# Optimization experiments

Measured on AMD Instinct MI355X. Metric: run time of the kernel, lower is better.

The kernel has to match this reference:

```python
import jax, jax.numpy as jnp
import numpy as np

DIM = 1024
N_EXPERTS = 8
TOP_K = 2
EXPERT_HIDDEN = DIM * 2
B, T = 4, 4096


def setup_inputs() -> dict:
    key = jax.random.key(0)
    ks = jax.random.split(key, 5)
    # xavier_uniform with gain=0.02 for w1/w2 (fan_in=DIM, fan_out=EXPERT_HIDDEN)
    lim12 = 0.02 * np.sqrt(6.0 / (DIM + EXPERT_HIDDEN))
    lim3 = 0.02 * np.sqrt(6.0 / (EXPERT_HIDDEN + DIM))
    x = jax.random.normal(ks[0], (B, T, DIM), dtype=jnp.float32)
    router_w = 0.02 * jax.random.normal(ks[1], (N_EXPERTS, DIM), dtype=jnp.float32)
    w1 = jax.random.uniform(ks[2], (N_EXPERTS, DIM, EXPERT_HIDDEN), minval=-lim12, maxval=lim12, dtype=jnp.float32)
    w2 = jax.random.uniform(ks[3], (N_EXPERTS, DIM, EXPERT_HIDDEN), minval=-lim12, maxval=lim12, dtype=jnp.float32)
    w3 = jax.random.uniform(ks[4], (N_EXPERTS, EXPERT_HIDDEN, DIM), minval=-lim3, maxval=lim3, dtype=jnp.float32)
    return {"x": x, "router_w": router_w, "w1": w1, "w2": w2, "w3": w3}


def reference(x, router_w, w1, w2, w3):
    # Router: top-k softmax gating, renormalized over the selected k.
    logits = jnp.einsum('btd,ed->bte', x, router_w)          # [B,T,E]
    probs = jax.nn.softmax(logits, axis=-1)
    topk_vals, topk_idx = jax.lax.top_k(probs, TOP_K)        # [B,T,K]
    topk_weights = topk_vals / topk_vals.sum(axis=-1, keepdims=True)

    out = jnp.zeros_like(x)
    for e in range(N_EXPERTS):
        # gate weight for expert e per token (0 if e not in token's top-k)
        w_e = jnp.where(topk_idx == e, topk_weights, 0.0).sum(axis=-1)  # [B,T]
        h = jax.nn.silu(jnp.einsum('btd,dh->bth', x, w1[e])) * jnp.einsum('btd,dh->bth', x, w2[e])
        out = out + jnp.einsum('bth,hd->btd', h, w3[e]) * w_e[..., None]
    aux_loss = jnp.float32(0.0)  # eval mode
    return (out, aux_loss)
```

## Files before the change

kernel.cpp:

```cpp
#include <hip/hip_runtime.h>
#include <stdint.h>

#define TTOK 16384
#define NDIM 1024
#define NHID 2048
#define NEXP 8
#define TM 256
#define MAXT 136
#define SLOTCAP (2 * TTOK + NEXP * TM)

typedef __attribute__((ext_vector_type(8))) short short8;
typedef __attribute__((ext_vector_type(4))) float f32x4;

__device__ __forceinline__ unsigned short f2bf(float f) {
  unsigned int u = __float_as_uint(f);
  u += 0x7FFFu + ((u >> 16) & 1u);
  return (unsigned short)(u >> 16);
}

__device__ __forceinline__ void gload16(const void* g, void* l) {
  __builtin_amdgcn_global_load_lds(
      (const __attribute__((address_space(1))) unsigned int*)g,
      (__attribute__((address_space(3))) unsigned int*)l, 16, 0, 0);
}

__device__ __forceinline__ float silu(float z) {
  return z / (1.0f + __expf(-z));
}

__device__ __forceinline__ void router_block(int b, const float* __restrict__ x,
                                             const float* __restrict__ rw,
                                             unsigned short* __restrict__ xbf,
                                             int* __restrict__ tok_e,
                                             float* __restrict__ tok_gw) {
  int t = (b << 2) + (threadIdx.x >> 6);
  int lane = threadIdx.x & 63;
  const float4* xr = (const float4*)(x + (size_t)t * NDIM);

  float4 v[4];
  float d[NEXP];
#pragma unroll
  for (int e = 0; e < NEXP; ++e) d[e] = 0.f;

#pragma unroll
  for (int i = 0; i < 4; ++i) {
    int c = i * 64 + lane;
    v[i] = xr[c];
#pragma unroll
    for (int e = 0; e < NEXP; ++e) {
      float4 w = ((const float4*)(rw + e * NDIM))[c];
      d[e] += v[i].x * w.x + v[i].y * w.y + v[i].z * w.z + v[i].w * w.w;
    }
  }
#pragma unroll
  for (int e = 0; e < NEXP; ++e)
    for (int s = 32; s; s >>= 1) d[e] += __shfl_xor(d[e], s, 64);

  unsigned short* xo = xbf + (size_t)t * NDIM;
#pragma unroll
  for (int i = 0; i < 4; ++i) {
    int c = i * 64 + lane;
    ushort4 u;
    u.x = f2bf(v[i].x); u.y = f2bf(v[i].y); u.z = f2bf(v[i].z); u.w = f2bf(v[i].w);
    ((ushort4*)xo)[c] = u;
  }

  if (lane == 0) {
    float m = d[0];
#pragma unroll
    for (int e = 1; e < NEXP; ++e) m = fmaxf(m, d[e]);
    float ex[NEXP];
#pragma unroll
    for (int e = 0; e < NEXP; ++e) ex[e] = __expf(d[e] - m);
    int e0 = 0;
#pragma unroll
    for (int e = 1; e < NEXP; ++e) if (ex[e] > ex[e0]) e0 = e;
    int e1 = (e0 == 0) ? 1 : 0;
#pragma unroll
    for (int e = 0; e < NEXP; ++e) if (e != e0 && ex[e] > ex[e1]) e1 = e;
    float p0 = ex[e0], p1 = ex[e1];
    float inv = 1.f / (p0 + p1);
    tok_e[2 * t] = e0; tok_e[2 * t + 1] = e1;
    tok_gw[2 * t] = p0 * inv; tok_gw[2 * t + 1] = p1 * inv;
  }
}

__device__ __forceinline__ void tconv_tile(const float* __restrict__ src,
                                           unsigned short* __restrict__ dst,
                                           int R, int C, int bx, int by) {
  __shared__ unsigned short tile[64][65];
  int tx = threadIdx.x & 15, ty = threadIdx.x >> 4;
#pragma unroll
  for (int rr = 0; rr < 4; ++rr) {
    int rl = rr * 16 + ty;
    float4 v = *(const float4*)(src + (size_t)(by + rl) * C + bx + tx * 4);
    tile[rl][tx * 4 + 0] = f2bf(v.x);
    tile[rl][tx * 4 + 1] = f2bf(v.y);
    tile[rl][tx * 4 + 2] = f2bf(v.z);
    tile[rl][tx * 4 + 3] = f2bf(v.w);
  }
  __syncthreads();
#pragma unroll
  for (int rr = 0; rr < 4; ++rr) {
    int cl = rr * 16 + ty;
    ushort4 u;
    u.x = tile[tx * 4 + 0][cl];
    u.y = tile[tx * 4 + 1][cl];
    u.z = tile[tx * 4 + 2][cl];
    u.w = tile[tx * 4 + 3][cl];
    *(ushort4*)(dst + (size_t)(bx + cl) * R + by + tx * 4) = u;
  }
}

__global__ void k_prep(const float* __restrict__ x, const float* __restrict__ rw,
                       unsigned short* __restrict__ xbf, int* __restrict__ tok_e,
                       float* __restrict__ tok_gw, const float* __restrict__ w1,
                       const float* __restrict__ w2, const float* __restrict__ w3,
                       unsigned short* __restrict__ w1t, unsigned short* __restrict__ w2t,
                       unsigned short* __restrict__ w3t) {
  int b = blockIdx.x;
  if (b < 4096) {
    router_block(b, x, rw, xbf, tok_e, tok_gw);
    return;
  }
  int tcb = b - 4096;
  int bx = tcb & 31;
  int by = (tcb >> 5) & 15;
  int z = tcb >> 9;
  if (z < 16) {
    int e = z & 7;
    const float* src = (z < 8 ? w1 : w2) + (size_t)e * NDIM * NHID;
    unsigned short* dst = (z < 8 ? w1t : w2t) + (size_t)e * NDIM * NHID;
    tconv_tile(src, dst, NDIM, NHID, bx * 64, by * 64);
  } else {
    int e = z - 16;
    const float* src = w3 + (size_t)e * NHID * NDIM;
    unsigned short* dst = w3t + (size_t)e * NHID * NDIM;
    tconv_tile(src, dst, NHID, NDIM, by * 64, bx * 64);
  }
}

__global__ void k_count(const int* __restrict__ tok_e, unsigned int* __restrict__ counts) {
  __shared__ unsigned int h[NEXP];
  int tid = threadIdx.x;
  if (tid < NEXP) h[tid] = 0u;
  __syncthreads();
  for (int i = blockIdx.x * 256 + tid; i < 2 * TTOK; i += gridDim.x * 256)
    atomicAdd(&h[tok_e[i]], 1u);
  __syncthreads();
  if (tid < NEXP) atomicAdd(&counts[tid], h[tid]);
}

__global__ void k_offsets(const unsigned int* __restrict__ counts,
                          unsigned int* __restrict__ slotbase, unsigned int* __restrict__ cnt2,
                          unsigned int* __restrict__ tile_e, unsigned int* __restrict__ tile_m0) {
  int l = threadIdx.x;
  unsigned int c[NEXP], base[NEXP], tb[NEXP];
  unsigned int b = 0, t = 0;
#pragma unroll
  for (int e = 0; e < NEXP; ++e) {
    c[e] = counts[e];
    base[e] = b; tb[e] = t;
    unsigned int nt = (c[e] + TM - 1) / TM;
    b += nt * TM; t += nt;
  }
  if (l < NEXP) { slotbase[l] = base[l]; cnt2[l] = 0u; }
  for (int idx = l; idx < MAXT; idx += 64) {
    unsigned int te = 0xFFFFFFFFu, tm = 0;
#pragma unroll
    for (int e = 0; e < NEXP; ++e) {
      unsigned int nt = (c[e] + TM - 1) / TM;
      if ((unsigned)idx >= tb[e] && (unsigned)idx < tb[e] + nt) {
        te = (unsigned)e; tm = base[e] + ((unsigned)idx - tb[e]) * TM;
      }
    }
    tile_e[idx] = te; tile_m0[idx] = tm;
  }
}

__global__ void k_fill(const int* __restrict__ tok_e, const float* __restrict__ tok_gw,
                       const unsigned int* __restrict__ slotbase, unsigned int* __restrict__ cnt2,
                       unsigned int* __restrict__ tok_list, float* __restrict__ gate_list) {
  __shared__ unsigned int hcnt[NEXP];
  __shared__ unsigned int hbase[NEXP];
  int tid = threadIdx.x;
  int t = blockIdx.x * 256 + tid;
  if (tid < NEXP) hcnt[tid] = 0u;
  __syncthreads();
  int e0 = tok_e[2 * t], e1 = tok_e[2 * t + 1];
  float g0 = tok_gw[2 * t], g1 = tok_gw[2 * t + 1];
  unsigned int p0 = atomicAdd(&hcnt[e0], 1u);
  unsigned int p1 = atomicAdd(&hcnt[e1], 1u);
  __syncthreads();
  if (tid < NEXP) hbase[tid] = atomicAdd(&cnt2[tid], hcnt[tid]);
  __syncthreads();
  unsigned int s0 = slotbase[e0] + hbase[e0] + p0;
  unsigned int s1 = slotbase[e1] + hbase[e1] + p1;
  tok_list[s0] = (unsigned)t; gate_list[s0] = g0;
  tok_list[s1] = (unsigned)t; gate_list[s1] = g1;
}

__global__ void k_sentinel(float* __restrict__ out, float v) {
  if (threadIdx.x == 0 && blockIdx.x == 0) out[0] = v;
}

__global__ __launch_bounds__(512, 2) void k_gemm12(
    const unsigned short* __restrict__ xbf, const unsigned short* __restrict__ w1t,
    const unsigned short* __restrict__ w2t, unsigned short* __restrict__ H,
    const unsigned int* __restrict__ tok_list, const unsigned int* __restrict__ tile_e,
    const unsigned int* __restrict__ tile_m0) {
  unsigned int e = tile_e[blockIdx.y];
  if (e > 7u) return;
  int m0 = (int)tile_m0[blockIdx.y];
  int n0 = blockIdx.x * 128;

  __shared__ unsigned short As[2][256 * 64];
  __shared__ unsigned short B1s[2][128 * 64];
  __shared__ unsigned short B2s[2][128 * 64];

  int tid = threadIdx.x, w = tid >> 6, l = tid & 63;
  int rsub = tid >> 3;
  int swb = ((tid & 7) * 16) ^ ((rsub & 7) << 4);

  const unsigned short* aS[4];
#pragma unroll
  for (int jj = 0; jj < 4; ++jj) {
    int row = jj * 64 + rsub;
    aS[jj] = xbf + (size_t)tok_list[m0 + row] * NDIM + (swb >> 1);
  }
  const unsigned short* b1S[2];
  const unsigned short* b2S[2];
#pragma unroll
  for (int jj = 0; jj < 2; ++jj) {
    int row = jj * 64 + rsub;
    size_t off = ((size_t)e * NHID + n0 + row) * NDIM + (swb >> 1);
    b1S[jj] = w1t + off;
    b2S[jj] = w2t + off;
  }
  int ldsb = w * 1024;

  f32x4 acc1[8][2], acc2[8][2];
#pragma unroll
  for (int m = 0; m < 8; ++m)
#pragma unroll
    for (int n = 0; n < 2; ++n) { acc1[m][n] = (f32x4)0.f; acc2[m][n] = (f32x4)0.f; }

  int wr = (w >> 2) * 128, wc = (w & 3) * 32;

#pragma unroll
  for (int jj = 0; jj < 4; ++jj)
    gload16(aS[jj], (char*)As[0] + jj * 8192 + ldsb);
#pragma unroll
  for (int jj = 0; jj < 2; ++jj) {
    gload16(b1S[jj], (char*)B1s[0] + jj * 8192 + ldsb);
    gload16(b2S[jj], (char*)B2s[0] + jj * 8192 + ldsb);
  }

  for (int t = 0; t < 16; ++t) {
    int cur = t & 1, nxt = cur ^ 1;
    int keN = (t + 1) * 64;
    bool st = (t < 15);
    const char* A = (const char*)As[cur];
    const char* B1 = (const char*)B1s[cur];
    const char* B2 = (const char*)B2s[cur];
    char* An = (char*)As[nxt];
    char* B1n = (char*)B1s[nxt];
    char* B2n = (char*)B2s[nxt];

    asm volatile("s_waitcnt vmcnt(0)" ::: "memory");
    __builtin_amdgcn_s_barrier();
    __builtin_amdgcn_sched_barrier(0);

    if (st) {
#pragma unroll
      for (int jj = 0; jj < 4; ++jj)
        gload16(aS[jj] + keN, An + jj * 8192 + ldsb);
#pragma unroll
      for (int jj = 0; jj < 2; ++jj) {
        gload16(b1S[jj] + keN, B1n + jj * 8192 + ldsb);
        gload16(b2S[jj] + keN, B2n + jj * 8192 + ldsb);
      }
    }

    short8 ar[8], b1r[4], b2r[4];

#pragma unroll
    for (int ks = 0; ks < 2; ++ks) {
      int kb = ks * 64 + ((l >> 4) << 4);
#pragma unroll
      for (int m = 0; m < 4; ++m) {
        int r = wr + m * 16 + (l & 15);
        ar[ks * 4 + m] = *(const short8*)(A + r * 128 + (kb ^ ((r & 7) << 4)));
      }
#pragma unroll
      for (int n = 0; n < 2; ++n) {
        int r = wc + n * 16 + (l & 15);
        b1r[ks * 2 + n] = *(const short8*)(B1 + r * 128 + (kb ^ ((r & 7) << 4)));
      }
    }
    __builtin_amdgcn_s_barrier();
    __builtin_amdgcn_s_setprio(1);
#pragma unroll
    for (int ks = 0; ks < 2; ++ks)
#pragma unroll
      for (int m = 0; m < 4; ++m)
#pragma unroll
        for (int n = 0; n < 2; ++n)
          acc1[m][n] = __builtin_amdgcn_mfma_f32_16x16x32_bf16(ar[ks * 4 + m], b1r[ks * 2 + n],
                                                              acc1[m][n], 0, 0, 0);
    __builtin_amdgcn_s_setprio(0);

#pragma unroll
    for (int ks = 0; ks < 2; ++ks) {
      int kb = ks * 64 + ((l >> 4) << 4);
#pragma unroll
      for (int n = 0; n < 2; ++n) {
        int r = wc + n * 16 + (l & 15);
        b2r[ks * 2 + n] = *(const short8*)(B2 + r * 128 + (kb ^ ((r & 7) << 4)));
      }
    }
    __builtin_amdgcn_s_barrier();
    __builtin_amdgcn_s_setprio(1);
#pragma unroll
    for (int ks = 0; ks < 2; ++ks)
#pragma unroll
      for (int m = 0; m < 4; ++m)
#pragma unroll
        for (int n = 0; n < 2; ++n)
          acc2[m][n] = __builtin_amdgcn_mfma_f32_16x16x32_bf16(ar[ks * 4 + m], b2r[ks * 2 + n],
                                                              acc2[m][n], 0, 0, 0);
    __builtin_amdgcn_s_setprio(0);

#pragma unroll
    for (int ks = 0; ks < 2; ++ks) {
      int kb = ks * 64 + ((l >> 4) << 4);
#pragma unroll
      for (int m = 0; m < 4; ++m) {
        int r = wr + 64 + m * 16 + (l & 15);
        ar[ks * 4 + m] = *(const short8*)(A + r * 128 + (kb ^ ((r & 7) << 4)));
      }
    }
    __builtin_amdgcn_s_barrier();
    __builtin_amdgcn_s_setprio(1);
#pragma unroll
    for (int ks = 0; ks < 2; ++ks)
#pragma unroll
      for (int m = 0; m < 4; ++m)
#pragma unroll
        for (int n = 0; n < 2; ++n)
          acc1[4 + m][n] = __builtin_amdgcn_mfma_f32_16x16x32_bf16(ar[ks * 4 + m], b1r[ks * 2 + n],
                                                                  acc1[4 + m][n], 0, 0, 0);
    __builtin_amdgcn_s_setprio(0);

    __builtin_amdgcn_s_barrier();
    __builtin_amdgcn_s_setprio(1);
#pragma unroll
    for (int ks = 0; ks < 2; ++ks)
#pragma unroll
      for (int m = 0; m < 4; ++m)
#pragma unroll
        for (int n = 0; n < 2; ++n)
          acc2[4 + m][n] = __builtin_amdgcn_mfma_f32_16x16x32_bf16(ar[ks * 4 + m], b2r[ks * 2 + n],
                                                                  acc2[4 + m][n], 0, 0, 0);
    __builtin_amdgcn_s_setprio(0);
  }

#pragma unroll
  for (int m = 0; m < 8; ++m)
#pragma unroll
    for (int n = 0; n < 2; ++n) {
      int col = n0 + wc + n * 16 + (l & 15);
#pragma unroll
      for (int q = 0; q < 4; ++q) {
        int slot = m0 + wr + m * 16 + ((l >> 4) << 2) + q;
        float hv = silu(acc1[m][n][q]) * acc2[m][n][q];
        H[(size_t)slot * NHID + col] = f2bf(hv);
      }
    }
}

__global__ __launch_bounds__(256, 2) void k_gemm3(
    const unsigned short* __restrict__ H, const unsigned short* __restrict__ w3t,
    float* __restrict__ out, const unsigned int* __restrict__ tok_list,
    const float* __restrict__ gate_list, const unsigned int* __restrict__ tile_e,
    const unsigned int* __restrict__ tile_m0) {
  unsigned int e = tile_e[blockIdx.y >> 1];
  if (e > 7u) return;
  int m0 = (int)tile_m0[blockIdx.y >> 1] + (int)(blockIdx.y & 1) * 128;
  int n0 = blockIdx.x * 128;

  __shared__ unsigned short As[128 * 64];
  __shared__ unsigned short Bs[128 * 64];

  int tid = threadIdx.x, w = tid >> 6, l = tid & 63;
  int rsub = tid >> 3;
  int swb = ((tid & 7) * 16) ^ ((rsub & 7) << 4);

  const unsigned short* aS[4];
  const unsigned short* bS[4];
#pragma unroll
  for (int jj = 0; jj < 4; ++jj) {
    int row = jj * 32 + rsub;
    aS[jj] = H + (size_t)(m0 + row) * NHID + (swb >> 1);
    bS[jj] = w3t + ((size_t)e * NDIM + n0 + row) * NHID + (swb >> 1);
  }
  int ldsb = w * 1024;

  f32x4 acc[4][4];
#pragma unroll
  for (int m = 0; m < 4; ++m)
#pragma unroll
    for (int n = 0; n < 4; ++n) acc[m][n] = (f32x4)0.f;

  int wr = (w >> 1) * 64, wc = (w & 1) * 64;

  for (int t = 0; t < 32; ++t) {
    int ke = t * 64;
#pragma unroll
    for (int jj = 0; jj < 4; ++jj) {
      gload16(aS[jj] + ke, (char*)As + jj * 4096 + ldsb);
      gload16(bS[jj] + ke, (char*)Bs + jj * 4096 + ldsb);
    }
    __syncthreads();
#pragma unroll
    for (int ks = 0; ks < 2; ++ks) {
      int kb = ks * 64 + ((l >> 4) << 4);
      short8 a[4], b[4];
#pragma unroll
      for (int m = 0; m < 4; ++m) {
        int r = wr + m * 16 + (l & 15);
        a[m] = *(const short8*)((const char*)As + r * 128 + (kb ^ ((r & 7) << 4)));
      }
#pragma unroll
      for (int n = 0; n < 4; ++n) {
        int r = wc + n * 16 + (l & 15);
        b[n] = *(const short8*)((const char*)Bs + r * 128 + (kb ^ ((r & 7) << 4)));
      }
#pragma unroll
      for (int m = 0; m < 4; ++m)
#pragma unroll
        for (int n = 0; n < 4; ++n)
          acc[m][n] = __builtin_amdgcn_mfma_f32_16x16x32_bf16(a[m], b[n], acc[m][n], 0, 0, 0);
    }
    __syncthreads();
  }

#pragma unroll
  for (int m = 0; m < 4; ++m)
#pragma unroll
    for (int q = 0; q < 4; ++q) {
      int slot = m0 + wr + m * 16 + ((l >> 4) << 2) + q;
      unsigned int tok = tok_list[slot];
      float g = gate_list[slot];
      if (g != 0.f) {
        float* orow = out + (size_t)tok * NDIM + n0 + wc;
#pragma unroll
        for (int n = 0; n < 4; ++n)
          atomicAdd(orow + n * 16 + (l & 15), acc[m][n][q] * g);
      }
    }
}

extern "C" void kernel_launch(void* const* d_in, const int* in_sizes, int n_in,
                              void* d_out, int out_size, void* d_ws, size_t ws_size,
                              hipStream_t stream) {
  const float* x = (const float*)d_in[0];
  const float* rw = (const float*)d_in[1];
  const float* w1 = (const float*)d_in[2];
  const float* w2 = (const float*)d_in[3];
  const float* w3 = (const float*)d_in[4];
  float* out = (float*)d_out;
  char* ws = (char*)d_ws;

  size_t o = 0;
  auto alloc = [&](size_t b) { size_t r = o; o = (o + b + 255) & ~(size_t)255; return r; };
  size_t o_xbf = alloc((size_t)TTOK * NDIM * 2);
  size_t o_w3t = alloc((size_t)NEXP * NDIM * NHID * 2);
  size_t o_H = alloc((size_t)SLOTCAP * NHID * 2);
  size_t o_tok = alloc((size_t)SLOTCAP * 4);
  size_t o_gate = alloc((size_t)SLOTCAP * 4);
  size_t o_te = alloc((size_t)TTOK * 2 * 4);
  size_t o_tg = alloc((size_t)TTOK * 2 * 4);
  size_t o_cnt = alloc(64);
  size_t o_cnt2 = alloc(64);
  size_t o_sb = alloc(64);
  size_t o_tle = alloc(MAXT * 4 + 64);
  size_t o_tlm = alloc(MAXT * 4 + 64);
  size_t need = o;

  size_t outBytes = (size_t)out_size * sizeof(float);
  size_t wtBytes = (size_t)NEXP * NDIM * NHID * 2;

  if (ws_size < need || outBytes < 2 * wtBytes) {
    hipMemsetAsync(d_out, 0, outBytes, stream);
    k_sentinel<<<1, 64, 0, stream>>>(out, (float)((double)ws_size / 1048576.0));
    return;
  }

  unsigned short* xbf = (unsigned short*)(ws + o_xbf);
  unsigned short* w3t = (unsigned short*)(ws + o_w3t);
  unsigned short* Hbuf = (unsigned short*)(ws + o_H);
  unsigned int* tok_list = (unsigned int*)(ws + o_tok);
  float* gate_list = (float*)(ws + o_gate);
  int* tok_e = (int*)(ws + o_te);
  float* tok_gw = (float*)(ws + o_tg);
  unsigned int* counts = (unsigned int*)(ws + o_cnt);
  unsigned int* cnt2 = (unsigned int*)(ws + o_cnt2);
  unsigned int* slotbase = (unsigned int*)(ws + o_sb);
  unsigned int* tile_e = (unsigned int*)(ws + o_tle);
  unsigned int* tile_m0 = (unsigned int*)(ws + o_tlm);

  unsigned short* w1t = (unsigned short*)d_out;
  unsigned short* w2t = (unsigned short*)((char*)d_out + wtBytes);

  hipMemsetAsync(counts, 0, 64, stream);
  hipMemsetAsync(tok_list, 0, (size_t)SLOTCAP * 4, stream);
  hipMemsetAsync(gate_list, 0, (size_t)SLOTCAP * 4, stream);

  k_prep<<<16384, 256, 0, stream>>>(x, rw, xbf, tok_e, tok_gw, w1, w2, w3, w1t, w2t, w3t);
  k_count<<<64, 256, 0, stream>>>(tok_e, counts);
  k_offsets<<<1, 64, 0, stream>>>(counts, slotbase, cnt2, tile_e, tile_m0);
  k_fill<<<TTOK / 256, 256, 0, stream>>>(tok_e, tok_gw, slotbase, cnt2, tok_list, gate_list);

  k_gemm12<<<dim3(NHID / 128, MAXT), 512, 0, stream>>>(xbf, w1t, w2t, Hbuf, tok_list,
                                                       tile_e, tile_m0);

  hipMemsetAsync(d_out, 0, outBytes, stream);

  k_gemm3<<<dim3(NDIM / 128, 2 * MAXT), 256, 0, stream>>>(Hbuf, w3t, out, tok_list, gate_list,
                                                          tile_e, tile_m0);
}
```

Before: 724.5 us.

## Interleave chunked prefetch with MFMA phases using partial vmcnt waits

Splits each K-step's global-to-LDS prefetch into four chunks (A halves, B1, B2). Each chunk is issued just before the compute phase that no longer needs its buffer, and the full vmcnt(0) wait is replaced by partial waits that block only on the data the next phase reads. The final iteration is peeled off, so the loop needs no conditional store. This is meant to hide load latency behind the MFMA phases rather than stalling on every load at the top of each iteration. The cost is more complex counter bookkeeping, which breaks if the load order changes.

Result: faster. 690.8 us (-4.7%).

```diff
diff --git a/kernel.cpp b/kernel.cpp
--- a/kernel.cpp
+++ b/kernel.cpp
@@ -247,19 +247,83 @@
 
   int wr = (w >> 2) * 128, wc = (w & 3) * 32;
 
-#pragma unroll
-  for (int jj = 0; jj < 4; ++jj)
-    gload16(aS[jj], (char*)As[0] + jj * 8192 + ldsb);
-#pragma unroll
-  for (int jj = 0; jj < 2; ++jj) {
-    gload16(b1S[jj], (char*)B1s[0] + jj * 8192 + ldsb);
-    gload16(b2S[jj], (char*)B2s[0] + jj * 8192 + ldsb);
-  }
-
-  for (int t = 0; t < 16; ++t) {
+  short8 ar[8], b1r[4], b2r[4];
+
+  auto rdA_mh0_B1 = [&](const char* A, const char* B1) {
+#pragma unroll
+    for (int ks = 0; ks < 2; ++ks) {
+      int kb = ks * 64 + ((l >> 4) << 4);
+#pragma unroll
+      for (int m = 0; m < 4; ++m) {
+        int r = wr + m * 16 + (l & 15);
+        ar[ks * 4 + m] = *(const short8*)(A + r * 128 + (kb ^ ((r & 7) << 4)));
+      }
+#pragma unroll
+      for (int n = 0; n < 2; ++n) {
+        int r = wc + n * 16 + (l & 15);
+        b1r[ks * 2 + n] = *(const short8*)(B1 + r * 128 + (kb ^ ((r & 7) << 4)));
+      }
+    }
+  };
+  auto rdB2 = [&](const char* B2) {
+#pragma unroll
+    for (int ks = 0; ks < 2; ++ks) {
+      int kb = ks * 64 + ((l >> 4) << 4);
+#pragma unroll
+      for (int n = 0; n < 2; ++n) {
+        int r = wc + n * 16 + (l & 15);
+        b2r[ks * 2 + n] = *(const short8*)(B2 + r * 128 + (kb ^ ((r & 7) << 4)));
+      }
+    }
+  };
+  auto rdA_mh1 = [&](const char* A) {
+#pragma unroll
+    for (int ks = 0; ks < 2; ++ks) {
+      int kb = ks * 64 + ((l >> 4) << 4);
+#pragma unroll
+      for (int m = 0; m < 4; ++m) {
+        int r = wr + 64 + m * 16 + (l & 15);
+        ar[ks * 4 + m] = *(const short8*)(A + r * 128 + (kb ^ ((r & 7) << 4)));
+      }
+    }
+  };
+  auto mfma1 = [&](int mh) {
+    __builtin_amdgcn_s_setprio(1);
+#pragma unroll
+    for (int ks = 0; ks < 2; ++ks)
+#pragma unroll
+      for (int m = 0; m < 4; ++m)
+#pragma unroll
+        for (int n = 0; n < 2; ++n)
+          acc1[mh * 4 + m][n] = __builtin_amdgcn_mfma_f32_16x16x32_bf16(
+              ar[ks * 4 + m], b1r[ks * 2 + n], acc1[mh * 4 + m][n], 0, 0, 0);
+    __builtin_amdgcn_s_setprio(0);
+  };
+  auto mfma2 = [&](int mh) {
+    __builtin_amdgcn_s_setprio(1);
+#pragma unroll
+    for (int ks = 0; ks < 2; ++ks)
+#pragma unroll
+      for (int m = 0; m < 4; ++m)
+#pragma unroll
+        for (int n = 0; n < 2; ++n)
+          acc2[mh * 4 + m][n] = __builtin_amdgcn_mfma_f32_16x16x32_bf16(
+              ar[ks * 4 + m], b2r[ks * 2 + n], acc2[mh * 4 + m][n], 0, 0, 0);
+    __builtin_amdgcn_s_setprio(0);
+  };
+
+  gload16(aS[0], (char*)As[0] + 0 * 8192 + ldsb);
+  gload16(aS[2], (char*)As[0] + 2 * 8192 + ldsb);
+  gload16(b1S[0], (char*)B1s[0] + 0 * 8192 + ldsb);
+  gload16(b1S[1], (char*)B1s[0] + 1 * 8192 + ldsb);
+  gload16(aS[1], (char*)As[0] + 1 * 8192 + ldsb);
+  gload16(aS[3], (char*)As[0] + 3 * 8192 + ldsb);
+  gload16(b2S[0], (char*)B2s[0] + 0 * 8192 + ldsb);
+  gload16(b2S[1], (char*)B2s[0] + 1 * 8192 + ldsb);
+
+  for (int t = 0; t < 15; ++t) {
     int cur = t & 1, nxt = cur ^ 1;
     int keN = (t + 1) * 64;
-    bool st = (t < 15);
     const char* A = (const char*)As[cur];
     const char* B1 = (const char*)B1s[cur];
     const char* B2 = (const char*)B2s[cur];
@@ -267,102 +331,47 @@
     char* B1n = (char*)B1s[nxt];
     char* B2n = (char*)B2s[nxt];
 
+    gload16(aS[0] + keN, An + 0 * 8192 + ldsb);
+    gload16(aS[2] + keN, An + 2 * 8192 + ldsb);
+    asm volatile("s_waitcnt vmcnt(6)" ::: "memory");
+    __builtin_amdgcn_s_barrier();
+    rdA_mh0_B1(A, B1);
+    mfma1(0);
+    gload16(b1S[0] + keN, B1n + 0 * 8192 + ldsb);
+    gload16(b1S[1] + keN, B1n + 1 * 8192 + ldsb);
+    asm volatile("s_waitcnt vmcnt(4)" ::: "memory");
+    __builtin_amdgcn_s_barrier();
+    rdB2(B2);
+    mfma2(0);
+    gload16(aS[1] + keN, An + 1 * 8192 + ldsb);
+    gload16(aS[3] + keN, An + 3 * 8192 + ldsb);
+    asm volatile("s_waitcnt vmcnt(6)" ::: "memory");
+    __builtin_amdgcn_s_barrier();
+    rdA_mh1(A);
+    mfma1(1);
+    gload16(b2S[0] + keN, B2n + 0 * 8192 + ldsb);
+    gload16(b2S[1] + keN, B2n + 1 * 8192 + ldsb);
+    __builtin_amdgcn_s_barrier();
+    mfma2(1);
+  }
+
+  {
+    const char* A = (const char*)As[1];
+    const char* B1 = (const char*)B1s[1];
+    const char* B2 = (const char*)B2s[1];
+    asm volatile("s_waitcnt vmcnt(4)" ::: "memory");
+    __builtin_amdgcn_s_barrier();
+    rdA_mh0_B1(A, B1);
+    mfma1(0);
     asm volatile("s_waitcnt vmcnt(0)" ::: "memory");
     __builtin_amdgcn_s_barrier();
-    __builtin_amdgcn_sched_barrier(0);
-
-    if (st) {
-#pragma unroll
-      for (int jj = 0; jj < 4; ++jj)
-        gload16(aS[jj] + keN, An + jj * 8192 + ldsb);
-#pragma unroll
-      for (int jj = 0; jj < 2; ++jj) {
-        gload16(b1S[jj] + keN, B1n + jj * 8192 + ldsb);
-        gload16(b2S[jj] + keN, B2n + jj * 8192 + ldsb);
-      }
-    }
-
-    short8 ar[8], b1r[4], b2r[4];
-
-#pragma unroll
-    for (int ks = 0; ks < 2; ++ks) {
-      int kb = ks * 64 + ((l >> 4) << 4);
-#pragma unroll
-      for (int m = 0; m < 4; ++m) {
-        int r = wr + m * 16 + (l & 15);
-        ar[ks * 4 + m] = *(const short8*)(A + r * 128 + (kb ^ ((r & 7) << 4)));
-      }
-#pragma unroll
-      for (int n = 0; n < 2; ++n) {
-        int r = wc + n * 16 + (l & 15);
-        b1r[ks * 2 + n] = *(const short8*)(B1 + r * 128 + (kb ^ ((r & 7) << 4)));
-      }
-    }
-    __builtin_amdgcn_s_barrier();
-    __builtin_amdgcn_s_setprio(1);
-#pragma unroll
-    for (int ks = 0; ks < 2; ++ks)
-#pragma unroll
-      for (int m = 0; m < 4; ++m)
-#pragma unroll
-        for (int n = 0; n < 2; ++n)
-          acc1[m][n] = __builtin_amdgcn_mfma_f32_16x16x32_bf16(ar[ks * 4 + m], b1r[ks * 2 + n],
-                                                              acc1[m][n], 0, 0, 0);
-    __builtin_amdgcn_s_setprio(0);
-
-#pragma unroll
-    for (int ks = 0; ks < 2; ++ks) {
-      int kb = ks * 64 + ((l >> 4) << 4);
-#pragma unroll
-      for (int n = 0; n < 2; ++n) {
-        int r = wc + n * 16 + (l & 15);
-        b2r[ks * 2 + n] = *(const short8*)(B2 + r * 128 + (kb ^ ((r & 7) << 4)));
-      }
-    }
-    __builtin_amdgcn_s_barrier();
-    __builtin_amdgcn_s_setprio(1);
-#pragma unroll
-    for (int ks = 0; ks < 2; ++ks)
-#pragma unroll
-      for (int m = 0; m < 4; ++m)
-#pragma unroll
-        for (int n = 0; n < 2; ++n)
-          acc2[m][n] = __builtin_amdgcn_mfma_f32_16x16x32_bf16(ar[ks * 4 + m], b2r[ks * 2 + n],
-                                                              acc2[m][n], 0, 0, 0);
-    __builtin_amdgcn_s_setprio(0);
-
-#pragma unroll
-    for (int ks = 0; ks < 2; ++ks) {
-      int kb = ks * 64 + ((l >> 4) << 4);
-#pragma unroll
-      for (int m = 0; m < 4; ++m) {
-        int r = wr + 64 + m * 16 + (l & 15);
-        ar[ks * 4 + m] = *(const short8*)(A + r * 128 + (kb ^ ((r & 7) << 4)));
-      }
-    }
-    __builtin_amdgcn_s_barrier();
-    __builtin_amdgcn_s_setprio(1);
-#pragma unroll
-    for (int ks = 0; ks < 2; ++ks)
-#pragma unroll
-      for (int m = 0; m < 4; ++m)
-#pragma unroll
-        for (int n = 0; n < 2; ++n)
-          acc1[4 + m][n] = __builtin_amdgcn_mfma_f32_16x16x32_bf16(ar[ks * 4 + m], b1r[ks * 2 + n],
-                                                                  acc1[4 + m][n], 0, 0, 0);
-    __builtin_amdgcn_s_setprio(0);
-
-    __builtin_amdgcn_s_barrier();
-    __builtin_amdgcn_s_setprio(1);
-#pragma unroll
-    for (int ks = 0; ks < 2; ++ks)
-#pragma unroll
-      for (int m = 0; m < 4; ++m)
-#pragma unroll
-        for (int n = 0; n < 2; ++n)
-          acc2[4 + m][n] = __builtin_amdgcn_mfma_f32_16x16x32_bf16(ar[ks * 4 + m], b2r[ks * 2 + n],
-                                                                  acc2[4 + m][n], 0, 0, 0);
-    __builtin_amdgcn_s_setprio(0);
+    rdB2(B2);
+    mfma2(0);
+    __builtin_amdgcn_s_barrier();
+    rdA_mh1(A);
+    mfma1(1);
+    __builtin_amdgcn_s_barrier();
+    mfma2(1);
   }
 
 #pragma unroll
```
